# Optimization experiments

Measured on AMD Instinct MI355X. Metric: run time of the kernel, lower is better.

## Reference

```python
import jax, jax.numpy as jnp
import numpy as np

N_TYPES = 4
NEG_SLOPE = 0.01


def _conv(x, row, col, edge_type, edge_weight, W, b):
    # x: [N, d_in], W: [4, d_in, d_out], b: [d_out]
    N = x.shape[0]
    # in-degree based symmetric normalization (deg counted on col, as in source)
    deg = jax.ops.segment_sum(jnp.ones(col.shape[0], dtype=x.dtype), col, num_segments=N)
    deg_inv_sqrt = jnp.where(deg > 0, deg ** -0.5, jnp.zeros((), x.dtype))
    norm = deg_inv_sqrt[row] * deg_inv_sqrt[col] * edge_weight  # [E]
    # project all nodes by each of the 4 relation weights, then gather per edge
    # (equivalent to per-edge bmm x[col] @ W[edge_type], but avoids [E,d,d])
    xw = jnp.einsum('ni,tio->tno', x, W)          # [4, N, d_out]
    x_j = xw[edge_type, col] * norm[:, None]      # [E, d_out]
    out = jax.ops.segment_sum(x_j, row, num_segments=N) + b  # [N, d_out]
    # dropout omitted (eval mode / deterministic reference)
    return jax.nn.leaky_relu(out, negative_slope=NEG_SLOPE)


def setup_inputs() -> dict:
    key = jax.random.key(0)
    ks = jax.random.split(key, 10)
    N, d, E = 50000, 128, 625000
    x = jax.random.normal(ks[0], (N, d), dtype=jnp.float32)
    edge_index = jax.random.randint(ks[1], (2, E), 0, N, dtype=jnp.int64 if jax.config.jax_enable_x64 else jnp.int32)
    edge_type = jax.random.randint(ks[2], (E,), 0, N_TYPES)
    edge_attr = jax.random.uniform(ks[3], (E,), dtype=jnp.float32)
    # xavier_uniform for (4, d, d): gain=1, bound = sqrt(6/(d+d))
    bound = float(np.sqrt(6.0 / (d + d)))
    W1 = jax.random.uniform(ks[4], (N_TYPES, d, d), minval=-bound, maxval=bound, dtype=jnp.float32)
    W2 = jax.random.uniform(ks[5], (N_TYPES, d, d), minval=-bound, maxval=bound, dtype=jnp.float32)
    W3 = jax.random.uniform(ks[6], (N_TYPES, d, d), minval=-bound, maxval=bound, dtype=jnp.float32)
    b1 = jnp.zeros((d,), jnp.float32)
    b2 = jnp.zeros((d,), jnp.float32)
    b3 = jnp.zeros((d,), jnp.float32)
    return {"x": x, "edge_index": edge_index, "edge_type": edge_type, "edge_attr": edge_attr,
            "W1": W1, "b1": b1, "W2": W2, "b2": b2, "W3": W3, "b3": b3}


def reference(x, edge_index, edge_type, edge_attr, W1, b1, W2, b2, W3, b3):
    row, col = edge_index[0], edge_index[1]
    z1 = _conv(x, row, col, edge_type, edge_attr, W1, b1)
    z2 = _conv(z1, row, col, edge_type, edge_attr, W2, b2)
    z3 = _conv(z2, row, col, edge_type, edge_attr, W3, b3)
    return (x + z1 + z2 + z3) / 4
```

## Files before the change

### kernel.cpp

```cpp
#include <hip/hip_runtime.h>

#define DIM 128
#define SLOTS 64

typedef __attribute__((ext_vector_type(8))) short bf16x8;
typedef __attribute__((ext_vector_type(4))) float f32x4;
typedef unsigned short u16;
typedef unsigned int u32;
typedef unsigned long long u64;

__device__ __forceinline__ float bf2f(u32 u) {
    return __builtin_bit_cast(float, u << 16);
}
__device__ __forceinline__ u16 f2bf(float f) {
    u32 u = __builtin_bit_cast(u32, f);
    u = (u + 0x7FFFu + ((u >> 16) & 1u)) >> 16;
    return (u16)u;
}
__device__ __forceinline__ u32 pack2bf(float a, float b) {
    return (u32)f2bf(a) | ((u32)f2bf(b) << 16);
}


__global__ __launch_bounds__(256) void k_setup(const int* __restrict__ row, const int* __restrict__ col,
                                               const int* __restrict__ et, const float* __restrict__ ew,
                                               int E, int* __restrict__ deg, int* __restrict__ fill,
                                               u64* __restrict__ ep,
                                               const float* __restrict__ x, u16* __restrict__ xb, int nx4,
                                               const float* __restrict__ W1, const float* __restrict__ W2,
                                               const float* __restrict__ W3,
                                               u16* __restrict__ Wt1, u16* __restrict__ Wt2,
                                               u16* __restrict__ Wt3, int nEb, int nXb) {
    int b = blockIdx.x, tid = threadIdx.x;
    if (b < nEb) {
        int e0 = (b * 256 + tid) * 4;
        #pragma unroll
        for (int i = 0; i < 4; i++) {
            int e = e0 + i;
            if (e < E) {
                int r = row[e], c = col[e];
                atomicAdd(&deg[c], 1);
                int pos = atomicAdd(&fill[r], 1);
                if (pos < SLOTS)
                    ep[(size_t)r * SLOTS + pos] =
                        ((u64)__builtin_bit_cast(u32, ew[e]) << 32) | (u32)((c << 8) | et[e]);
            }
        }
    } else if (b < nEb + nXb) {
        int i = (b - nEb) * 256 + tid;
        if (i < nx4) {
            float4 v = ((const float4*)x)[i];
            ushort4 o;
            o.x = f2bf(v.x); o.y = f2bf(v.y); o.z = f2bf(v.z); o.w = f2bf(v.w);
            ((ushort4*)xb)[i] = o;
        }
    } else {
        int b2 = b - nEb - nXb;
        const float* W = b2 < 256 ? W1 : (b2 < 512 ? W2 : W3);
        u16* Wt = b2 < 256 ? Wt1 : (b2 < 512 ? Wt2 : Wt3);
        int o = (b2 & 255) * 256 + tid;
        int chunk = o >> 10;
        int c = (o >> 3) & 127;
        int k = chunk * 8 + (o & 7);
        Wt[o] = f2bf(W[(k >> 7) * 16384 + (k & 127) * 128 + c]);
    }
}


__global__ __launch_bounds__(256) void k_norm(const int* __restrict__ fill,
                                              const int* __restrict__ deg,
                                              u64* __restrict__ ep, int N) {
    int wid = threadIdx.x >> 6, lane = threadIdx.x & 63;
    int n = blockIdx.x * 4 + wid;
    if (n >= N) return;
    int cnt = fill[n]; if (cnt > SLOTS) cnt = SLOTS;
    int padded = (cnt + 7) & ~7;
    int dgn = deg[n];
    float dn = dgn > 0 ? rsqrtf((float)dgn) : 0.f;
    u64* eb = ep + (size_t)n * SLOTS;
    if (lane < cnt) {
        u64 q = eb[lane];
        u32 lo = (u32)q;
        int dgc = deg[lo >> 8];
        float dc = dgc > 0 ? rsqrtf((float)dgc) : 0.f;
        float wgt = __builtin_bit_cast(float, (u32)(q >> 32)) * dn * dc;
        eb[lane] = ((u64)__builtin_bit_cast(u32, wgt) << 32) | lo;
    } else if (lane < padded) {
        eb[lane] = 0;
    }
}


template <int MODE>
__global__ __launch_bounds__(1024, 2) void k_layer(const u16* __restrict__ src,
                                                   const int* __restrict__ fill,
                                                   const u64* __restrict__ ep,
                                                   const u16* __restrict__ Wt,
                                                   const float* __restrict__ bias,
                                                   const float* __restrict__ x0,
                                                   const u16* __restrict__ z1b,
                                                   const u16* __restrict__ z2b,
                                                   float* __restrict__ outf,
                                                   u16* __restrict__ outb, int N) {
    __shared__ u16 sA[16 * 512];
    int tid = threadIdx.x, wid = tid >> 6, lane = tid & 63;
    int n0 = blockIdx.x * 16;
    int n = n0 + wid;

    float2 a0 = {0.f, 0.f}, a1 = {0.f, 0.f}, a2 = {0.f, 0.f}, a3 = {0.f, 0.f};
    int cnt = 0;
    if (n < N) {
        cnt = fill[n];
        if (cnt > SLOTS) cnt = SLOTS;
    }
    const u64* eb = ep + (size_t)n * SLOTS;
    const char* xbase = (const char*)src + lane * 4;

#define RFL(x) __builtin_amdgcn_readfirstlane((int)(x))

#define EDGE(lo_, wu_, v_) { \
        float w_  = __builtin_bit_cast(float, (u32)(wu_)); \
        float vl_ = __builtin_bit_cast(float, (v_) << 16); \
        float vh_ = __builtin_bit_cast(float, (v_) & 0xFFFF0000u); \
        u32 t_ = (u32)(lo_) & 3u; \
        float w0_ = t_ == 0u ? w_ : 0.f; \
        float w1_ = t_ == 1u ? w_ : 0.f; \
        float w2_ = t_ == 2u ? w_ : 0.f; \
        float w3_ = t_ == 3u ? w_ : 0.f; \
        a0.x = fmaf(vl_, w0_, a0.x); a0.y = fmaf(vh_, w0_, a0.y); \
        a1.x = fmaf(vl_, w1_, a1.x); a1.y = fmaf(vh_, w1_, a1.y); \
        a2.x = fmaf(vl_, w2_, a2.x); a2.y = fmaf(vh_, w2_, a2.y); \
        a3.x = fmaf(vl_, w3_, a3.x); a3.y = fmaf(vh_, w3_, a3.y); }

    for (int j = 0; j < cnt; j += 8) {
        const uint4* ebv = (const uint4*)(eb + j);
        uint4 qa = ebv[0], qb = ebv[1], qc = ebv[2], qd = ebv[3];
        u32 lo0 = (u32)RFL(qa.x), wu0 = (u32)RFL(qa.y);
        u32 lo1 = (u32)RFL(qa.z), wu1 = (u32)RFL(qa.w);
        u32 lo2 = (u32)RFL(qb.x), wu2 = (u32)RFL(qb.y);
        u32 lo3 = (u32)RFL(qb.z), wu3 = (u32)RFL(qb.w);
        u32 lo4 = (u32)RFL(qc.x), wu4 = (u32)RFL(qc.y);
        u32 lo5 = (u32)RFL(qc.z), wu5 = (u32)RFL(qc.w);
        u32 lo6 = (u32)RFL(qd.x), wu6 = (u32)RFL(qd.y);
        u32 lo7 = (u32)RFL(qd.z), wu7 = (u32)RFL(qd.w);
        u32 v0 = *(const u32*)(xbase + (lo0 & 0xFFFFFF00u));
        u32 v1 = *(const u32*)(xbase + (lo1 & 0xFFFFFF00u));
        u32 v2 = *(const u32*)(xbase + (lo2 & 0xFFFFFF00u));
        u32 v3 = *(const u32*)(xbase + (lo3 & 0xFFFFFF00u));
        u32 v4 = *(const u32*)(xbase + (lo4 & 0xFFFFFF00u));
        u32 v5 = *(const u32*)(xbase + (lo5 & 0xFFFFFF00u));
        u32 v6 = *(const u32*)(xbase + (lo6 & 0xFFFFFF00u));
        u32 v7 = *(const u32*)(xbase + (lo7 & 0xFFFFFF00u));
        EDGE(lo0, wu0, v0); EDGE(lo1, wu1, v1);
        EDGE(lo2, wu2, v2); EDGE(lo3, wu3, v3);
        EDGE(lo4, wu4, v4); EDGE(lo5, wu5, v5);
        EDGE(lo6, wu6, v6); EDGE(lo7, wu7, v7);
    }
#undef EDGE
#undef RFL

    {
        u32 X = (u32)((wid & 7) << 4);
        char* base = (char*)sA + wid * 1024;
        *(u32*)(base + ((lane * 4 + 0  ) ^ X)) = pack2bf(a0.x, a0.y);
        *(u32*)(base + ((lane * 4 + 256) ^ X)) = pack2bf(a1.x, a1.y);
        *(u32*)(base + ((lane * 4 + 512) ^ X)) = pack2bf(a2.x, a2.y);
        *(u32*)(base + ((lane * 4 + 768) ^ X)) = pack2bf(a3.x, a3.y);
    }
    __syncthreads();

    if (wid < 8) {
        int lr = lane & 15, lk = lane >> 4;
        u32 X = (u32)((lr & 7) << 4);
        const char* ab = (const char*)sA + lr * 1024;
        const u16* bb = Wt + lk * 1024 + (wid * 16 + lr) * 8;
        f32x4 acc = {};
        #pragma unroll
        for (int ks = 0; ks < 16; ks++) {
            bf16x8 af = *(const bf16x8*)(ab + ((ks * 64 + lk * 16) ^ X));
            bf16x8 bfv = *(const bf16x8*)(bb + ks * 4096);
            acc = __builtin_amdgcn_mfma_f32_16x16x32_bf16(af, bfv, acc, 0, 0, 0);
        }

        int colg = wid * 16 + lr;
        float bv = bias[colg];
        #pragma unroll
        for (int r = 0; r < 4; r++) {
            int nn = n0 + lk * 4 + r;
            if (nn < N) {
                size_t idx = (size_t)nn * DIM + colg;
                float v = acc[r] + bv;
                v = v > 0.f ? v : 0.01f * v;
                if (MODE == 1)
                    outf[idx] = 0.25f * (x0[idx] + bf2f(z1b[idx]) + bf2f(z2b[idx]) + v);
                else
                    outb[idx] = f2bf(v);
            }
        }
    }
}


extern "C" void kernel_launch(void* const* d_in, const int* in_sizes, int n_in,
                              void* d_out, int out_size, void* d_ws, size_t ws_size,
                              hipStream_t stream) {
    const float* x     = (const float*)d_in[0];
    const int*   eidx  = (const int*)d_in[1];
    const int*   etype = (const int*)d_in[2];
    const float* eattr = (const float*)d_in[3];
    const float* W1 = (const float*)d_in[4];
    const float* b1 = (const float*)d_in[5];
    const float* W2 = (const float*)d_in[6];
    const float* b2 = (const float*)d_in[7];
    const float* W3 = (const float*)d_in[8];
    const float* b3 = (const float*)d_in[9];

    const int E = in_sizes[2];
    const int N = in_sizes[0] / DIM;
    const int* row = eidx;
    const int* col = eidx + E;

    char* w = (char*)d_ws;
    size_t off = 0;
    auto alloc = [&](size_t bytes) { size_t o = off; off = (off + bytes + 255) & ~255ULL; return o; };
    size_t deg_off = alloc((size_t)N * 4);
    int*   deg  = (int*)(w + deg_off);
    int*   fill = (int*)(w + alloc((size_t)N * 4));
    size_t zero_bytes = off - deg_off;
    u64*   ep   = (u64*)(w + alloc((size_t)N * SLOTS * 8));
    u16*   xb   = (u16*)(w + alloc((size_t)N * DIM * 2));
    u16*   z1b  = (u16*)(w + alloc((size_t)N * DIM * 2));
    u16*   z2b  = (u16*)(w + alloc((size_t)N * DIM * 2));
    u16*   Wt1  = (u16*)(w + alloc(65536 * 2));
    u16*   Wt2  = (u16*)(w + alloc(65536 * 2));
    u16*   Wt3  = (u16*)(w + alloc(65536 * 2));

    hipMemsetAsync(deg, 0, zero_bytes, stream);

    int nx4 = N * DIM / 4;
    int nEb = (E + 1023) / 1024;
    int nXb = (nx4 + 255) / 256;

    k_setup<<<nEb + nXb + 768, 256, 0, stream>>>(row, col, etype, eattr, E, deg, fill, ep,
                                                 x, xb, nx4, W1, W2, W3, Wt1, Wt2, Wt3, nEb, nXb);
    k_norm<<<(N + 3) / 4, 256, 0, stream>>>(fill, deg, ep, N);

    int grid = (N + 15) / 16;
    k_layer<0><<<grid, 1024, 0, stream>>>(xb,  fill, ep, Wt1, b1, nullptr, nullptr, nullptr, nullptr, z1b, N);
    k_layer<0><<<grid, 1024, 0, stream>>>(z1b, fill, ep, Wt2, b2, nullptr, nullptr, nullptr, nullptr, z2b, N);
    k_layer<1><<<grid, 1024, 0, stream>>>(z2b, fill, ep, Wt3, b3, x, z1b, z2b, (float*)d_out, nullptr, N);
}
```

Baseline: 235.8 us.

## Software-pipeline edge-slot loads and feature gathers across rounds in aggregation loop

Restructures the per-node edge aggregation loop into a two-stage software pipeline. Edge descriptors for the next round, and the gathers for the following group of 8 edges, are issued before the current group's FMAs are consumed, so memory latency overlaps with math. The cost is more live registers (double-buffered descriptors and gathered values), which may reduce occupancy. The loop also prefetches one round past cnt, which stays inside the fixed 64-slot buffer.

Measured after the change: 267.0 us. 13.2% more time.

```diff
diff --git a/kernel.cpp b/kernel.cpp
--- a/kernel.cpp
+++ b/kernel.cpp
@@ -113,50 +113,76 @@
         cnt = fill[n];
         if (cnt > SLOTS) cnt = SLOTS;
     }
-    const u64* eb = ep + (size_t)n * SLOTS;
+    const uint4* ebv = (const uint4*)(ep + (size_t)n * SLOTS);
     const char* xbase = (const char*)src + lane * 4;
 
 #define RFL(x) __builtin_amdgcn_readfirstlane((int)(x))
-
-#define EDGE(lo_, wu_, v_) { \
-        float w_  = __builtin_bit_cast(float, (u32)(wu_)); \
-        float vl_ = __builtin_bit_cast(float, (v_) << 16); \
-        float vh_ = __builtin_bit_cast(float, (v_) & 0xFFFF0000u); \
-        u32 t_ = (u32)(lo_) & 3u; \
-        float w0_ = t_ == 0u ? w_ : 0.f; \
-        float w1_ = t_ == 1u ? w_ : 0.f; \
-        float w2_ = t_ == 2u ? w_ : 0.f; \
-        float w3_ = t_ == 3u ? w_ : 0.f; \
-        a0.x = fmaf(vl_, w0_, a0.x); a0.y = fmaf(vh_, w0_, a0.y); \
-        a1.x = fmaf(vl_, w1_, a1.x); a1.y = fmaf(vh_, w1_, a1.y); \
-        a2.x = fmaf(vl_, w2_, a2.x); a2.y = fmaf(vh_, w2_, a2.y); \
-        a3.x = fmaf(vl_, w3_, a3.x); a3.y = fmaf(vh_, w3_, a3.y); }
-
-    for (int j = 0; j < cnt; j += 8) {
-        const uint4* ebv = (const uint4*)(eb + j);
-        uint4 qa = ebv[0], qb = ebv[1], qc = ebv[2], qd = ebv[3];
-        u32 lo0 = (u32)RFL(qa.x), wu0 = (u32)RFL(qa.y);
-        u32 lo1 = (u32)RFL(qa.z), wu1 = (u32)RFL(qa.w);
-        u32 lo2 = (u32)RFL(qb.x), wu2 = (u32)RFL(qb.y);
-        u32 lo3 = (u32)RFL(qb.z), wu3 = (u32)RFL(qb.w);
-        u32 lo4 = (u32)RFL(qc.x), wu4 = (u32)RFL(qc.y);
-        u32 lo5 = (u32)RFL(qc.z), wu5 = (u32)RFL(qc.w);
-        u32 lo6 = (u32)RFL(qd.x), wu6 = (u32)RFL(qd.y);
-        u32 lo7 = (u32)RFL(qd.z), wu7 = (u32)RFL(qd.w);
-        u32 v0 = *(const u32*)(xbase + (lo0 & 0xFFFFFF00u));
-        u32 v1 = *(const u32*)(xbase + (lo1 & 0xFFFFFF00u));
-        u32 v2 = *(const u32*)(xbase + (lo2 & 0xFFFFFF00u));
-        u32 v3 = *(const u32*)(xbase + (lo3 & 0xFFFFFF00u));
-        u32 v4 = *(const u32*)(xbase + (lo4 & 0xFFFFFF00u));
-        u32 v5 = *(const u32*)(xbase + (lo5 & 0xFFFFFF00u));
-        u32 v6 = *(const u32*)(xbase + (lo6 & 0xFFFFFF00u));
-        u32 v7 = *(const u32*)(xbase + (lo7 & 0xFFFFFF00u));
-        EDGE(lo0, wu0, v0); EDGE(lo1, wu1, v1);
-        EDGE(lo2, wu2, v2); EDGE(lo3, wu3, v3);
-        EDGE(lo4, wu4, v4); EDGE(lo5, wu5, v5);
-        EDGE(lo6, wu6, v6); EDGE(lo7, wu7, v7);
-    }
-#undef EDGE
+#define LOADB(Bx, r_) { const uint4* p_ = ebv + (r_) * 4; \
+        Bx[0] = p_[0]; Bx[1] = p_[1]; Bx[2] = p_[2]; Bx[3] = p_[3]; }
+#define DEC(LO, WU, Bx) { \
+        LO[0] = (u32)RFL(Bx[0].x); WU[0] = (u32)RFL(Bx[0].y); \
+        LO[1] = (u32)RFL(Bx[0].z); WU[1] = (u32)RFL(Bx[0].w); \
+        LO[2] = (u32)RFL(Bx[1].x); WU[2] = (u32)RFL(Bx[1].y); \
+        LO[3] = (u32)RFL(Bx[1].z); WU[3] = (u32)RFL(Bx[1].w); \
+        LO[4] = (u32)RFL(Bx[2].x); WU[4] = (u32)RFL(Bx[2].y); \
+        LO[5] = (u32)RFL(Bx[2].z); WU[5] = (u32)RFL(Bx[2].w); \
+        LO[6] = (u32)RFL(Bx[3].x); WU[6] = (u32)RFL(Bx[3].y); \
+        LO[7] = (u32)RFL(Bx[3].z); WU[7] = (u32)RFL(Bx[3].w); }
+#define ISSUE(G, LO) { \
+        _Pragma("unroll") \
+        for (int i_ = 0; i_ < 8; i_++) \
+            G[i_] = *(const u32*)(xbase + (LO[i_] & 0xFFFFFF00u)); }
+#define CONS(G, LO, WU) { \
+        _Pragma("unroll") \
+        for (int i_ = 0; i_ < 8; i_++) { \
+            float w_  = __builtin_bit_cast(float, WU[i_]); \
+            float vl_ = __builtin_bit_cast(float, G[i_] << 16); \
+            float vh_ = __builtin_bit_cast(float, G[i_] & 0xFFFF0000u); \
+            u32 t_ = LO[i_] & 3u; \
+            float w0_ = t_ == 0u ? w_ : 0.f; \
+            float w1_ = t_ == 1u ? w_ : 0.f; \
+            float w2_ = t_ == 2u ? w_ : 0.f; \
+            float w3_ = t_ == 3u ? w_ : 0.f; \
+            a0.x = fmaf(vl_, w0_, a0.x); a0.y = fmaf(vh_, w0_, a0.y); \
+            a1.x = fmaf(vl_, w1_, a1.x); a1.y = fmaf(vh_, w1_, a1.y); \
+            a2.x = fmaf(vl_, w2_, a2.x); a2.y = fmaf(vh_, w2_, a2.y); \
+            a3.x = fmaf(vl_, w3_, a3.x); a3.y = fmaf(vh_, w3_, a3.y); } }
+
+    int rounds = (cnt + 7) >> 3;
+    if (rounds > 0) {
+        uint4 B0[4], B1[4];
+        u32 S0lo[8], S0wu[8], S1lo[8], S1wu[8];
+        u32 G0[8], G1[8];
+
+        LOADB(B0, 0);
+        DEC(S0lo, S0wu, B0);
+        LOADB(B1, 1);
+        ISSUE(G0, S0lo);
+
+        int k = 1;
+        for (; k + 1 < rounds; k += 2) {
+            DEC(S1lo, S1wu, B1);
+            LOADB(B0, k + 1);
+            ISSUE(G1, S1lo);
+            CONS(G0, S0lo, S0wu);
+            DEC(S0lo, S0wu, B0);
+            LOADB(B1, k + 2);
+            ISSUE(G0, S0lo);
+            CONS(G1, S1lo, S1wu);
+        }
+        if (k < rounds) {
+            DEC(S1lo, S1wu, B1);
+            ISSUE(G1, S1lo);
+            CONS(G0, S0lo, S0wu);
+            CONS(G1, S1lo, S1wu);
+        } else {
+            CONS(G0, S0lo, S0wu);
+        }
+    }
+#undef CONS
+#undef ISSUE
+#undef DEC
+#undef LOADB
 #undef RFL
 
     {
```
